# Performance work log

Hardware: AMD Instinct MI355X
Metric: run time of the kernel (lower is better)

Reference implementation:

```python
import jax, jax.numpy as jnp
import numpy as np


def _base_grid(B, H, W):
    xs = jnp.arange(W, dtype=jnp.float32)
    ys = jnp.arange(H, dtype=jnp.float32)
    gx, gy = jnp.meshgrid(xs, ys)  # [H,W] each, x varies along W
    return jnp.broadcast_to(jnp.stack([gx, gy], -1)[None], (B, H, W, 2))


def flow_to_grid(flow, accel=None):
    B, _, H, W = flow.shape
    v = 0.5 * flow
    if accel is not None:
        v = v + 0.25 * accel
    vgrid = _base_grid(B, H, W) + jnp.transpose(v, (0, 2, 3, 1))
    gx = 2.0 * vgrid[..., 0] / max(W - 1, 1) - 1.0
    gy = 2.0 * vgrid[..., 1] / max(H - 1, 1) - 1.0
    return jnp.stack([gx, gy], -1)  # [B,H,W,2]


def grid_sample_border(img, grid):
    # img [B,C,H,W], grid [B,Hg,Wg,2] normalized; bilinear, border pad, align_corners=True
    B, C, H, W = img.shape
    Hg, Wg = grid.shape[1], grid.shape[2]
    x = jnp.clip((grid[..., 0] + 1.0) * 0.5 * (W - 1), 0.0, W - 1)
    y = jnp.clip((grid[..., 1] + 1.0) * 0.5 * (H - 1), 0.0, H - 1)
    x0 = jnp.floor(x); y0 = jnp.floor(y)
    x1 = jnp.minimum(x0 + 1.0, W - 1); y1 = jnp.minimum(y0 + 1.0, H - 1)
    wx = (x - x0)[:, None]; wy = (y - y0)[:, None]  # [B,1,Hg,Wg]
    x0i, x1i, y0i, y1i = (a.astype(jnp.int32) for a in (x0, x1, y0, y1))
    flat = img.reshape(B, C, H * W)

    def gat(yi, xi):
        idx = jnp.broadcast_to((yi * W + xi).reshape(B, 1, Hg * Wg), (B, C, Hg * Wg))
        return jnp.take_along_axis(flat, idx, axis=2).reshape(B, C, Hg, Wg)

    v00, v01, v10, v11 = gat(y0i, x0i), gat(y0i, x1i), gat(y1i, x0i), gat(y1i, x1i)
    return v00 * (1 - wx) * (1 - wy) + v01 * wx * (1 - wy) + v10 * (1 - wx) * wy + v11 * wx * wy


def backward_warp(img, flow, accel=None):
    grid = flow_to_grid(flow, accel)
    warped = grid_sample_border(img, grid)
    valid = (jnp.abs(grid[..., 0]) <= 1.0) & (jnp.abs(grid[..., 1]) <= 1.0)
    return warped * valid[:, None].astype(img.dtype)


def local_kernel_warp(img, flow, kernel_params):
    B, C, H, W = img.shape
    k_row = jax.nn.softmax(kernel_params[:, :5], axis=1)   # [B,5,H,W]
    k_col = jax.nn.softmax(kernel_params[:, 5:10], axis=1)
    aniso = jax.nn.sigmoid(kernel_params[:, 10]) + 0.5     # [B,H,W]
    grid = flow_to_grid(flow)                               # [B,H,W,2]
    offsets = jnp.linspace(-2.0, 2.0, 5)
    a3 = aniso[..., None]                                   # [B,H,W,1]
    off_col = offsets.reshape(1, 1, 1, 5) * a3              # [B,H,W,5]
    off_row = offsets.reshape(1, 1, 1, 5) / a3
    zeros = jnp.zeros_like(off_row)
    grid_row = grid[:, :, :, None, :] + jnp.stack([off_row, zeros], -1) * (2.0 / W)
    samples_row = grid_sample_border(img, grid_row.reshape(B, H, W * 5, 2)).reshape(B, C, H, W, 5)
    img_row = jnp.einsum('bchwk,bkhw->bchw', samples_row, k_row)
    grid_base = flow_to_grid(jnp.zeros_like(flow))
    grid_col = grid_base[:, :, :, None, :] + jnp.stack([zeros, off_col], -1) * (2.0 / H)
    samples_col = grid_sample_border(img_row, grid_col.reshape(B, H, W * 5, 2)).reshape(B, C, H, W, 5)
    return jnp.einsum('bchwk,bkhw->bchw', samples_col, k_col)


def conv3x3(x, w, b):
    y = jax.lax.conv_general_dilated(x, w, (1, 1), 'SAME',
                                     dimension_numbers=('NCHW', 'OIHW', 'NCHW'))
    return y + b[None, :, None, None]


def reference(img, features, flow, kernel_params, w1, b1, w2, b2):
    B, _, H, W = img.shape
    Hf, Wf = features.shape[2], features.shape[3]
    warped_img = local_kernel_warp(img, flow, kernel_params)
    flow_scaled = jax.image.resize(flow, (B, 2, Hf, Wf), 'linear') * (Hf / H)
    warped_feat = backward_warp(features, flow_scaled)
    warped_img_down = jax.image.resize(warped_img, (B, 3, Hf, Wf), 'linear')
    x = jnp.concatenate([warped_feat, warped_img_down], axis=1)
    fused = conv3x3(jax.nn.relu(conv3x3(x, w1, b1)), w2, b2)
    return (warped_feat + fused, warped_img)


def setup_inputs() -> dict:
    key = jax.random.key(0)
    ks = jax.random.split(key, 6)
    B, H, W, Hf, Wf, Cf = 4, 512, 512, 256, 256, 96
    return {
        'img': jax.random.uniform(ks[0], (B, 3, H, W), jnp.float32),
        'features': jax.random.normal(ks[1], (B, Cf, Hf, Wf), jnp.float32),
        'flow': jax.random.normal(ks[2], (B, 2, H, W), jnp.float32) * 4.0,
        'kernel_params': jax.random.normal(ks[3], (B, 11, H, W), jnp.float32),
        'w1': jax.random.normal(ks[4], (Cf, Cf + 3, 3, 3), jnp.float32) * 0.02,
        'b1': jnp.zeros((Cf,), jnp.float32),
        'w2': jax.random.normal(ks[5], (Cf, Cf, 3, 3), jnp.float32) * 0.02,
        'b2': jnp.zeros((Cf,), jnp.float32),
    }
```

## Files before the change

kernel.cpp:

```cpp
#include <hip/hip_runtime.h>

#define NB 4
#define IH 512
#define IW 512
#define FH 256
#define FW 256
#define CF 96
#define C1 99
#define HWI (IH*IW)
#define HWF (FH*FW)

typedef short s8v __attribute__((ext_vector_type(8)));
typedef short s4v __attribute__((ext_vector_type(4)));
typedef float f4v __attribute__((ext_vector_type(4)));
typedef float f2v __attribute__((ext_vector_type(2), aligned(4)));

static __device__ __forceinline__ float sigmoidf_(float x) {
    return 1.0f / (1.0f + __expf(-x));
}
static __device__ __forceinline__ unsigned short f2bf(float f) {
    unsigned int u = __float_as_uint(f);
    unsigned int r = (u + 0x7fffu + ((u >> 16) & 1u)) >> 16;
    return (unsigned short)r;
}
static __device__ __forceinline__ float bf2f(short s) {
    unsigned int u = ((unsigned int)(unsigned short)s) << 16;
    return __uint_as_float(u);
}
static __device__ __forceinline__ void gl_lds16(const short* g, short* l) {
    __builtin_amdgcn_global_load_lds(
        (const __attribute__((address_space(1))) void*)g,
        (__attribute__((address_space(3))) void*)l, 16, 0, 0);
}

__global__ __launch_bounds__(256)
void lkw_row_kernel(const float* __restrict__ img,
                    const float* __restrict__ flow,
                    const float* __restrict__ kp,
                    float* __restrict__ img_row) {
    int idx = blockIdx.x * blockDim.x + threadIdx.x;
    if (idx >= NB * HWI) return;
    int w = idx & (IW - 1);
    int h = (idx >> 9) & (IH - 1);
    int b = idx >> 18;

    const float* kpb = kp + (size_t)b * 11 * HWI + h * IW + w;
    float p[5];
    float m = -1e30f;
    #pragma unroll
    for (int k = 0; k < 5; k++) { p[k] = kpb[k * HWI]; m = fmaxf(m, p[k]); }
    float s = 0.f;
    #pragma unroll
    for (int k = 0; k < 5; k++) { p[k] = __expf(p[k] - m); s += p[k]; }
    float invs = 1.f / s;
    float a = sigmoidf_(kpb[10 * HWI]) + 0.5f;
    float inva = 1.f / a;

    float fx = flow[((size_t)b * 2 + 0) * HWI + h * IW + w];
    float fy = flow[((size_t)b * 2 + 1) * HWI + h * IW + w];

    float y = (float)h + 0.5f * fy;
    y = fminf(fmaxf(y, 0.f), (float)(IH - 1));
    float y0f = floorf(y);
    int y0 = (int)y0f;
    int y1 = min(y0 + 1, IH - 1);
    float wy = y - y0f;

    float xbase = (float)w + 0.5f * fx;
    const float sc = (float)(IW - 1) / (float)IW;

    const float* imb = img + (size_t)b * 3 * HWI;
    float acc0 = 0.f, acc1 = 0.f, acc2 = 0.f;
    #pragma unroll
    for (int k = 0; k < 5; k++) {
        float x = xbase + (float)(k - 2) * inva * sc;
        x = fminf(fmaxf(x, 0.f), (float)(IW - 1));
        float x0f = floorf(x);
        int x0 = (int)x0f;
        int x1 = min(x0 + 1, IW - 1);
        float wx = x - x0f;
        float wk = p[k] * invs;
        float w00 = (1.f - wx) * (1.f - wy) * wk;
        float w01 = wx * (1.f - wy) * wk;
        float w10 = (1.f - wx) * wy * wk;
        float w11 = wx * wy * wk;
        int i00 = y0 * IW + x0, i01 = y0 * IW + x1;
        int i10 = y1 * IW + x0, i11 = y1 * IW + x1;
        acc0 += w00 * imb[i00] + w01 * imb[i01] + w10 * imb[i10] + w11 * imb[i11];
        acc1 += w00 * imb[HWI + i00] + w01 * imb[HWI + i01] + w10 * imb[HWI + i10] + w11 * imb[HWI + i11];
        acc2 += w00 * imb[2 * HWI + i00] + w01 * imb[2 * HWI + i01] + w10 * imb[2 * HWI + i10] + w11 * imb[2 * HWI + i11];
    }
    img_row[(size_t)b * 3 * HWI + h * IW + w] = acc0;
    img_row[(size_t)b * 3 * HWI + HWI + h * IW + w] = acc1;
    img_row[(size_t)b * 3 * HWI + 2 * HWI + h * IW + w] = acc2;
}

__global__ __launch_bounds__(256)
void lkw_col_kernel(const float* __restrict__ img_row,
                    const float* __restrict__ kp,
                    float* __restrict__ out1) {
    int idx = blockIdx.x * blockDim.x + threadIdx.x;
    if (idx >= NB * HWI) return;
    int w = idx & (IW - 1);
    int h = (idx >> 9) & (IH - 1);
    int b = idx >> 18;

    const float* kpb = kp + (size_t)b * 11 * HWI + h * IW + w;
    float p[5];
    float m = -1e30f;
    #pragma unroll
    for (int k = 0; k < 5; k++) { p[k] = kpb[(5 + k) * HWI]; m = fmaxf(m, p[k]); }
    float s = 0.f;
    #pragma unroll
    for (int k = 0; k < 5; k++) { p[k] = __expf(p[k] - m); s += p[k]; }
    float invs = 1.f / s;
    float a = sigmoidf_(kpb[10 * HWI]) + 0.5f;

    const float sc = (float)(IH - 1) / (float)IH;
    const float* irb = img_row + (size_t)b * 3 * HWI;
    float acc0 = 0.f, acc1 = 0.f, acc2 = 0.f;
    #pragma unroll
    for (int k = 0; k < 5; k++) {
        float y = (float)h + (float)(k - 2) * a * sc;
        y = fminf(fmaxf(y, 0.f), (float)(IH - 1));
        float y0f = floorf(y);
        int y0 = (int)y0f;
        int y1 = min(y0 + 1, IH - 1);
        float wy = y - y0f;
        float wk = p[k] * invs;
        float w0 = (1.f - wy) * wk, w1 = wy * wk;
        int i0 = y0 * IW + w, i1 = y1 * IW + w;
        acc0 += w0 * irb[i0] + w1 * irb[i1];
        acc1 += w0 * irb[HWI + i0] + w1 * irb[HWI + i1];
        acc2 += w0 * irb[2 * HWI + i0] + w1 * irb[2 * HWI + i1];
    }
    out1[(size_t)b * 3 * HWI + h * IW + w] = acc0;
    out1[(size_t)b * 3 * HWI + HWI + h * IW + w] = acc1;
    out1[(size_t)b * 3 * HWI + 2 * HWI + h * IW + w] = acc2;
}

static __device__ __forceinline__ void ds_taps(int i, int n_in, int t[4], float wt[4]) {
    int n_out = n_in >> 1;
    if (i == 0) {
        t[0] = 0; t[1] = 0; t[2] = 1; t[3] = 2;
        wt[0] = 0.f; wt[1] = 3.f / 7.f; wt[2] = 3.f / 7.f; wt[3] = 1.f / 7.f;
    } else if (i == n_out - 1) {
        t[0] = n_in - 3; t[1] = n_in - 2; t[2] = n_in - 1; t[3] = n_in - 1;
        wt[0] = 1.f / 7.f; wt[1] = 3.f / 7.f; wt[2] = 3.f / 7.f; wt[3] = 0.f;
    } else {
        t[0] = 2 * i - 1; t[1] = 2 * i; t[2] = 2 * i + 1; t[3] = 2 * i + 2;
        wt[0] = 0.125f; wt[1] = 0.375f; wt[2] = 0.375f; wt[3] = 0.125f;
    }
}

__global__ __launch_bounds__(256)
void downsample2x_kernel(const float* __restrict__ src, float* __restrict__ dst,
                         int BC, float mul) {
    int idx = blockIdx.x * blockDim.x + threadIdx.x;
    if (idx >= BC * HWF) return;
    int j = idx & (FW - 1);
    int i = (idx >> 8) & (FH - 1);
    int bc = idx >> 16;

    int tx[4], ty[4];
    float wx[4], wy[4];
    ds_taps(j, IW, tx, wx);
    ds_taps(i, IH, ty, wy);
    const float* s = src + (size_t)bc * HWI;
    float acc = 0.f;
    #pragma unroll
    for (int a = 0; a < 4; a++) {
        if (wy[a] == 0.f) continue;
        const float* rp = s + (size_t)ty[a] * IW;
        float row = wx[0] * rp[tx[0]] + wx[1] * rp[tx[1]] + wx[2] * rp[tx[2]] + wx[3] * rp[tx[3]];
        acc += wy[a] * row;
    }
    dst[idx] = acc * mul;
}

__global__ __launch_bounds__(256)
void imgdown_cl_kernel(const float* __restrict__ out1, short* __restrict__ xin) {
    int idx = blockIdx.x * blockDim.x + threadIdx.x;
    if (idx >= NB * HWF) return;
    int j = idx & (FW - 1);
    int i = (idx >> 8) & (FH - 1);
    int b = idx >> 16;

    int tx[4], ty[4];
    float wx[4], wy[4];
    ds_taps(j, IW, tx, wx);
    ds_taps(i, IH, ty, wy);
    const float* s = out1 + (size_t)b * 3 * HWI;
    float acc[3] = {0.f, 0.f, 0.f};
    #pragma unroll
    for (int a = 0; a < 4; a++) {
        if (wy[a] == 0.f) continue;
        #pragma unroll
        for (int c = 0; c < 3; c++) {
            const float* rp = s + (size_t)c * HWI + (size_t)ty[a] * IW;
            float row = wx[0] * rp[tx[0]] + wx[1] * rp[tx[1]] + wx[2] * rp[tx[2]] + wx[3] * rp[tx[3]];
            acc[c] += wy[a] * row;
        }
    }
    short* dst = xin + ((size_t)(b * FH + i) * FW + j) * 128 + 96;
    s8v g0 = { (short)f2bf(acc[0]), (short)f2bf(acc[1]), (short)f2bf(acc[2]), 0, 0, 0, 0, 0 };
    s8v z  = { 0, 0, 0, 0, 0, 0, 0, 0 };
    *(s8v*)(dst)      = g0;
    *(s8v*)(dst + 8)  = z;
    *(s8v*)(dst + 16) = z;
    *(s8v*)(dst + 24) = z;
}

template <int BF>
__global__ __launch_bounds__(256)
void feat_cl_kernel(const float* __restrict__ feat, void* __restrict__ featT) {
    __shared__ float tile[64 * 97];
    int blk = blockIdx.x;
    int b = blk >> 10;
    int p0 = (blk & 1023) << 6;
    int t = threadIdx.x;
    {
        int px = t & 63, cq = t >> 6;
        const float* src = feat + (size_t)b * CF * HWF + p0 + px;
        #pragma unroll
        for (int k = 0; k < 24; k++) {
            int c = cq * 24 + k;
            tile[px * 97 + c] = src[(size_t)c * HWF];
        }
    }
    __syncthreads();
    int pxo = t >> 2, co = (t & 3) * 24;
    const float* trow = &tile[pxo * 97 + co];
    size_t obase = ((size_t)(b * HWF) + p0 + pxo) * 96 + co;
    if (BF) {
        short* dst = (short*)featT + obase;
        #pragma unroll
        for (int q = 0; q < 3; q++) {
            s8v pk;
            #pragma unroll
            for (int e = 0; e < 8; e++) pk[e] = (short)f2bf(trow[q * 8 + e]);
            *(s8v*)(dst + q * 8) = pk;
        }
    } else {
        float* dst = (float*)featT + obase;
        #pragma unroll
        for (int q = 0; q < 6; q++) {
            f4v vv = { trow[q * 4 + 0], trow[q * 4 + 1], trow[q * 4 + 2], trow[q * 4 + 3] };
            *(f4v*)(dst + q * 4) = vv;
        }
    }
}

template <int BF>
__global__ __launch_bounds__(256)
void warp_feat_cl2_kernel(const void* __restrict__ featT,
                          const float* __restrict__ flow_s,
                          float* __restrict__ wfeat,
                          short* __restrict__ xin) {
    int t = blockIdx.x * 256 + threadIdx.x;
    int g = t & 7;
    int pix = t >> 3;
    int j = pix & (FW - 1);
    int i = (pix >> 8) & (FH - 1);
    int b = pix >> 16;

    float fx = flow_s[((size_t)b * 2 + 0) * HWF + i * FW + j];
    float fy = flow_s[((size_t)b * 2 + 1) * HWF + i * FW + j];
    float u = (float)j + 0.5f * fx;
    float v = (float)i + 0.5f * fy;
    bool valid = (u >= 0.f) && (u <= (float)(FW - 1)) && (v >= 0.f) && (v <= (float)(FH - 1));
    float x = fminf(fmaxf(u, 0.f), (float)(FW - 1));
    float y = fminf(fmaxf(v, 0.f), (float)(FH - 1));
    int x0 = min((int)x, FW - 2);
    int y0 = min((int)y, FH - 2);
    float wxf = x - (float)x0, wyf = y - (float)y0;
    float w00 = (1.f - wxf) * (1.f - wyf), w01 = wxf * (1.f - wyf);
    float w10 = (1.f - wxf) * wyf, w11 = wxf * wyf;
    if (!valid) { w00 = w01 = w10 = w11 = 0.f; }

    size_t base = ((size_t)(b * HWF) + (size_t)y0 * FW + x0) * 96 + g * 12;
    float vals[12];
    if (BF) {
        const short* fp = (const short*)featT + base;
        #pragma unroll
        for (int q = 0; q < 3; q++) {
            s4v a0 = *(const s4v*)(fp + q * 4);
            s4v a1 = *(const s4v*)(fp + 96 + q * 4);
            s4v a2 = *(const s4v*)(fp + 96 * FW + q * 4);
            s4v a3 = *(const s4v*)(fp + 96 * FW + 96 + q * 4);
            #pragma unroll
            for (int e = 0; e < 4; e++)
                vals[q * 4 + e] = w00 * bf2f(a0[e]) + w01 * bf2f(a1[e])
                                + w10 * bf2f(a2[e]) + w11 * bf2f(a3[e]);
        }
    } else {
        const float* fp = (const float*)featT + base;
        #pragma unroll
        for (int q = 0; q < 3; q++) {
            f4v a0 = *(const f4v*)(fp + q * 4);
            f4v a1 = *(const f4v*)(fp + 96 + q * 4);
            f4v a2 = *(const f4v*)(fp + 96 * FW + q * 4);
            f4v a3 = *(const f4v*)(fp + 96 * FW + 96 + q * 4);
            #pragma unroll
            for (int e = 0; e < 4; e++)
                vals[q * 4 + e] = w00 * a0[e] + w01 * a1[e] + w10 * a2[e] + w11 * a3[e];
        }
    }

    float* ob = wfeat + ((size_t)b * CF + g * 12) * HWF + (size_t)i * FW + j;
    #pragma unroll
    for (int k = 0; k < 12; k++) ob[(size_t)k * HWF] = vals[k];

    short* xr = xin + (size_t)pix * 128 + g * 12;
    #pragma unroll
    for (int q2 = 0; q2 < 3; q2++) {
        s4v pk = { (short)f2bf(vals[q2 * 4 + 0]), (short)f2bf(vals[q2 * 4 + 1]),
                   (short)f2bf(vals[q2 * 4 + 2]), (short)f2bf(vals[q2 * 4 + 3]) };
        *(s4v*)(xr + q2 * 4) = pk;
    }
}

__global__ __launch_bounds__(256)
void warp_feat_cl_kernel(const float* __restrict__ feat,
                         const float* __restrict__ flow_s,
                         float* __restrict__ wfeat,
                         short* __restrict__ xin) {
    int t = blockIdx.x * 256 + threadIdx.x;
    int g = t & 7;
    int pix = t >> 3;
    int j = pix & (FW - 1);
    int i = (pix >> 8) & (FH - 1);
    int b = pix >> 16;

    float fx = flow_s[((size_t)b * 2 + 0) * HWF + i * FW + j];
    float fy = flow_s[((size_t)b * 2 + 1) * HWF + i * FW + j];
    float u = (float)j + 0.5f * fx;
    float v = (float)i + 0.5f * fy;
    bool valid = (u >= 0.f) && (u <= (float)(FW - 1)) && (v >= 0.f) && (v <= (float)(FH - 1));
    float x = fminf(fmaxf(u, 0.f), (float)(FW - 1));
    float y = fminf(fmaxf(v, 0.f), (float)(FH - 1));
    int x0 = min((int)x, FW - 2);
    int y0 = min((int)y, FH - 2);
    float wxf = x - (float)x0, wyf = y - (float)y0;
    float w00 = (1.f - wxf) * (1.f - wyf), w01 = wxf * (1.f - wyf);
    float w10 = (1.f - wxf) * wyf, w11 = wxf * wyf;
    if (!valid) { w00 = w01 = w10 = w11 = 0.f; }

    const float* fb = feat + ((size_t)b * CF + g * 12) * HWF + (size_t)y0 * FW + x0;
    float vals[12];
    #pragma unroll
    for (int k = 0; k < 12; k++) {
        const float* p = fb + (size_t)k * HWF;
        f2v r0 = *(const f2v*)p;
        f2v r1 = *(const f2v*)(p + FW);
        vals[k] = w00 * r0.x + w01 * r0.y + w10 * r1.x + w11 * r1.y;
    }

    float* ob = wfeat + ((size_t)b * CF + g * 12) * HWF + (size_t)i * FW + j;
    #pragma unroll
    for (int k = 0; k < 12; k++) ob[(size_t)k * HWF] = vals[k];

    short* xr = xin + (size_t)pix * 128 + g * 12;
    #pragma unroll
    for (int q2 = 0; q2 < 3; q2++) {
        s4v pk = { (short)f2bf(vals[q2 * 4 + 0]), (short)f2bf(vals[q2 * 4 + 1]),
                   (short)f2bf(vals[q2 * 4 + 2]), (short)f2bf(vals[q2 * 4 + 3]) };
        *(s4v*)(xr + q2 * 4) = pk;
    }
}

__global__ __launch_bounds__(256)
void cvt_w1_kernel(const float* __restrict__ w1, short* __restrict__ wA1,
                   short* __restrict__ zpage) {
    int i = blockIdx.x * 256 + threadIdx.x;
    if (i < 128) zpage[i] = 0;
    if (i >= 4 * 3 * 3 * 96 * 32) return;
    int cl = i & 31;
    int co = (i >> 5) % 96;
    int rest = i / 3072;
    int dx = rest % 3;
    int dy = (rest / 3) % 3;
    int kc = rest / 9;
    int ci = kc * 32 + cl;
    float v = (ci < C1) ? w1[((size_t)co * C1 + ci) * 9 + dy * 3 + dx] : 0.f;
    wA1[i] = (short)f2bf(v);
}
__global__ __launch_bounds__(256)
void cvt_w2_kernel(const float* __restrict__ w2, short* __restrict__ wA2) {
    int i = blockIdx.x * 256 + threadIdx.x;
    if (i >= 3 * 3 * 3 * 96 * 32) return;
    int cl = i & 31;
    int co = (i >> 5) % 96;
    int rest = i / 3072;
    int dx = rest % 3;
    int dy = (rest / 3) % 3;
    int kc = rest / 9;
    wA2[i] = (short)f2bf(w2[((size_t)co * CF + kc * 32 + cl) * 9 + dy * 3 + dx]);
}

template <int PASS>
__global__ __launch_bounds__(256)
void conv_mfma4_kernel(const short* __restrict__ X,
                       const short* __restrict__ W,
                       const float* __restrict__ bias,
                       const short* __restrict__ zpage,
                       short* __restrict__ t1out,
                       float* __restrict__ out0) {
    constexpr int KSTR = (PASS == 1) ? 128 : 96;
    constexpr int KC = KSTR / 32;
    __shared__ short Als[320 * 32];
    __shared__ short Bls[192 * 32];

    const int bx = blockIdx.x;
    const int w0 = (bx & 1) * 128;
    const int h  = (bx >> 1) & (FH - 1);
    const int b  = bx >> 9;

    const int tid = threadIdx.x;
    const int lane = tid & 63;
    const int wv = tid >> 6;
    const int ln = lane & 15;
    const int q  = lane >> 4;

    f4v acc[6][2];
    #pragma unroll
    for (int mt = 0; mt < 6; mt++)
        #pragma unroll
        for (int nt = 0; nt < 2; nt++)
            acc[mt][nt] = (f4v){0.f, 0.f, 0.f, 0.f};

    const short* Xb = X + (size_t)(b * FH) * FW * KSTR;
    const int bpx = wv * 48 + (lane >> 2);
    const int bch = lane & 3;

    for (int kc = 0; kc < KC; ++kc) {
        for (int dy = 0; dy < 3; ++dy) {
            const int step = kc * 3 + dy;
            const int hy = h + dy - 1;
            const bool hok = (hy >= 0) && (hy < FH);
            const short* Xrow = Xb + (size_t)(hok ? hy : 0) * FW * KSTR + kc * 32;
            const short* Wstep = W + (size_t)step * 288 * 32;

            __syncthreads();
            #pragma unroll
            for (int k = 0; k < 5; k++) {
                int c = k * 4 + wv;
                const short* g = (c < 18) ? (Wstep + c * 512 + lane * 8) : zpage;
                gl_lds16(g, Als + c * 512);
            }
            #pragma unroll
            for (int k = 0; k < 3; k++) {
                int px = bpx + k * 16;
                int wp = w0 - 1 + px;
                bool ok = hok && (px < 130) && (wp >= 0) && (wp < FW);
                const short* g = ok ? (Xrow + (size_t)wp * KSTR + bch * 8) : zpage;
                gl_lds16(g, Bls + (wv * 48 + k * 16) * 32);
            }
            __syncthreads();

            #pragma unroll
            for (int dx = 0; dx < 3; ++dx) {
                s8v bfr0 = *(const s8v*)(Bls + (wv * 32 + ln + dx) * 32 + q * 8);
                s8v bfr1 = *(const s8v*)(Bls + (wv * 32 + 16 + ln + dx) * 32 + q * 8);
                #pragma unroll
                for (int mt = 0; mt < 6; ++mt) {
                    s8v afr = *(const s8v*)(Als + (dx * 96 + mt * 16 + ln) * 32 + q * 8);
                    acc[mt][0] = __builtin_amdgcn_mfma_f32_16x16x32_bf16(afr, bfr0, acc[mt][0], 0, 0, 0);
                    acc[mt][1] = __builtin_amdgcn_mfma_f32_16x16x32_bf16(afr, bfr1, acc[mt][1], 0, 0, 0);
                }
            }
        }
    }

    if (PASS == 1) {
        const size_t rowbase = (size_t)(b * FH + h) * FW;
        #pragma unroll
        for (int nt = 0; nt < 2; ++nt) {
            int pos = w0 + wv * 32 + nt * 16 + ln;
            short* dst = t1out + (rowbase + pos) * CF;
            #pragma unroll
            for (int mt = 0; mt < 6; ++mt) {
                int co0 = mt * 16 + q * 4;
                s4v pk;
                #pragma unroll
                for (int r = 0; r < 4; ++r) {
                    float v = acc[mt][nt][r] + bias[co0 + r];
                    pk[r] = (short)f2bf(fmaxf(v, 0.f));
                }
                *(s4v*)(dst + co0) = pk;
            }
        }
    } else {
        #pragma unroll
        for (int nt = 0; nt < 2; ++nt) {
            int pos = w0 + wv * 32 + nt * 16 + ln;
            #pragma unroll
            for (int mt = 0; mt < 6; ++mt) {
                int co0 = mt * 16 + q * 4;
                #pragma unroll
                for (int r = 0; r < 4; ++r) {
                    size_t o = (size_t)(b * CF + co0 + r) * HWF + (size_t)h * FW + pos;
                    out0[o] += acc[mt][nt][r] + bias[co0 + r];
                }
            }
        }
    }
}

extern "C" void kernel_launch(void* const* d_in, const int* in_sizes, int n_in,
                              void* d_out, int out_size, void* d_ws, size_t ws_size,
                              hipStream_t stream) {
    const float* img  = (const float*)d_in[0];
    const float* feat = (const float*)d_in[1];
    const float* flow = (const float*)d_in[2];
    const float* kp   = (const float*)d_in[3];
    const float* w1   = (const float*)d_in[4];
    const float* b1   = (const float*)d_in[5];
    const float* w2   = (const float*)d_in[6];
    const float* b2   = (const float*)d_in[7];

    float* out0 = (float*)d_out;
    float* out1 = out0 + (size_t)NB * CF * HWF;

    char* wsb = (char*)d_ws;
    short* wA1 = (short*)wsb;
    short* wA2 = (short*)(wsb + 221184);
    short* zpage = (short*)(wsb + 387072);
    short* xin = (short*)(wsb + 387328);
    const size_t off_after_xin = 387328 + 67108864;

    const size_t FEATT_F32 = (size_t)NB * HWF * 96 * 4;
    const size_t FEATT_BF16 = (size_t)NB * HWF * 96 * 2;
    const size_t FLOW_B = 2097152;
    const size_t need_f32 = off_after_xin + FLOW_B + FEATT_F32;
    const size_t need_b16 = off_after_xin + FLOW_B + FEATT_BF16;

    int n_img = NB * HWI;
    hipLaunchKernelGGL(cvt_w1_kernel, dim3((9 * 96 * 128 + 255) / 256), dim3(256), 0, stream, w1, wA1, zpage);
    hipLaunchKernelGGL(cvt_w2_kernel, dim3((9 * 96 * 96 + 255) / 256), dim3(256), 0, stream, w2, wA2);

    if (ws_size >= need_b16) {
        const bool f32ok = (ws_size >= need_f32);
        float* flow_s = (float*)(wsb + off_after_xin);
        char* region  = wsb + off_after_xin + FLOW_B;
        float* img_row = (float*)region;
        void*  featT   = (void*)region;
        short* t1cl    = (short*)region;

        hipLaunchKernelGGL(lkw_row_kernel, dim3((n_img + 255) / 256), dim3(256), 0, stream,
                           img, flow, kp, img_row);
        hipLaunchKernelGGL(lkw_col_kernel, dim3((n_img + 255) / 256), dim3(256), 0, stream,
                           img_row, kp, out1);
        hipLaunchKernelGGL(downsample2x_kernel, dim3((NB * 2 * HWF + 255) / 256), dim3(256), 0, stream,
                           flow, flow_s, NB * 2, 0.5f);
        hipLaunchKernelGGL(imgdown_cl_kernel, dim3((NB * HWF + 255) / 256), dim3(256), 0, stream,
                           out1, xin);
        if (f32ok) {
            hipLaunchKernelGGL((feat_cl_kernel<0>), dim3(NB * (HWF / 64)), dim3(256), 0, stream,
                               feat, featT);
            hipLaunchKernelGGL((warp_feat_cl2_kernel<0>), dim3(NB * HWF * 8 / 256), dim3(256), 0, stream,
                               featT, flow_s, out0, xin);
        } else {
            hipLaunchKernelGGL((feat_cl_kernel<1>), dim3(NB * (HWF / 64)), dim3(256), 0, stream,
                               feat, featT);
            hipLaunchKernelGGL((warp_feat_cl2_kernel<1>), dim3(NB * HWF * 8 / 256), dim3(256), 0, stream,
                               featT, flow_s, out0, xin);
        }
        hipLaunchKernelGGL((conv_mfma4_kernel<1>), dim3(NB * FH * 2), dim3(256), 0, stream,
                           xin, wA1, b1, zpage, t1cl, (float*)nullptr);
        hipLaunchKernelGGL((conv_mfma4_kernel<2>), dim3(NB * FH * 2), dim3(256), 0, stream,
                           t1cl, wA2, b2, zpage, (short*)nullptr, out0);
    } else {
        char* region = wsb + off_after_xin;
        short* t1cl    = (short*)region;
        float* img_row = (float*)region;
        float* flow_s  = (float*)(region + 16777216);

        hipLaunchKernelGGL(lkw_row_kernel, dim3((n_img + 255) / 256), dim3(256), 0, stream,
                           img, flow, kp, img_row);
        hipLaunchKernelGGL(lkw_col_kernel, dim3((n_img + 255) / 256), dim3(256), 0, stream,
                           img_row, kp, out1);
        hipLaunchKernelGGL(downsample2x_kernel, dim3((NB * 2 * HWF + 255) / 256), dim3(256), 0, stream,
                           flow, flow_s, NB * 2, 0.5f);
        hipLaunchKernelGGL(imgdown_cl_kernel, dim3((NB * HWF + 255) / 256), dim3(256), 0, stream,
                           out1, xin);
        hipLaunchKernelGGL(warp_feat_cl_kernel, dim3(NB * HWF * 8 / 256), dim3(256), 0, stream,
                           feat, flow_s, out0, xin);
        hipLaunchKernelGGL((conv_mfma4_kernel<1>), dim3(NB * FH * 2), dim3(256), 0, stream,
                           xin, wA1, b1, zpage, t1cl, (float*)nullptr);
        hipLaunchKernelGGL((conv_mfma4_kernel<2>), dim3(NB * FH * 2), dim3(256), 0, stream,
                           t1cl, wA2, b2, zpage, (short*)nullptr, out0);
    }
}
```

Baseline: 606.1 us.

## Double-buffer LDS tiles in MFMA conv kernel to overlap loads with compute

Restructures the conv inner loop into a flattened step loop with two LDS buffers for weights and input rows. The next step's global-to-LDS loads are issued before computing the current step, with explicit vmcnt waits and raw barriers, and wave priority is raised during the MFMA section. This is meant to hide global load latency behind matrix math, at the cost of doubling LDS per block, which may lower occupancy.

```diff
diff --git a/kernel.cpp b/kernel.cpp
--- a/kernel.cpp
+++ b/kernel.cpp
@@ -400,7 +400,7 @@
 
 template <int PASS>
 __global__ __launch_bounds__(256)
-void conv_mfma4_kernel(const short* __restrict__ X,
+void conv_mfma5_kernel(const short* __restrict__ X,
                        const short* __restrict__ W,
                        const float* __restrict__ bias,
                        const short* __restrict__ zpage,
@@ -408,8 +408,9 @@
                        float* __restrict__ out0) {
     constexpr int KSTR = (PASS == 1) ? 128 : 96;
     constexpr int KC = KSTR / 32;
-    __shared__ short Als[320 * 32];
-    __shared__ short Bls[192 * 32];
+    constexpr int NSTEP = KC * 3;
+    __shared__ short Als[2][320 * 32];
+    __shared__ short Bls[2][192 * 32];
 
     const int bx = blockIdx.x;
     const int w0 = (bx & 1) * 128;
@@ -433,43 +434,57 @@
     const int bpx = wv * 48 + (lane >> 2);
     const int bch = lane & 3;
 
-    for (int kc = 0; kc < KC; ++kc) {
-        for (int dy = 0; dy < 3; ++dy) {
-            const int step = kc * 3 + dy;
-            const int hy = h + dy - 1;
-            const bool hok = (hy >= 0) && (hy < FH);
-            const short* Xrow = Xb + (size_t)(hok ? hy : 0) * FW * KSTR + kc * 32;
-            const short* Wstep = W + (size_t)step * 288 * 32;
-
-            __syncthreads();
+    auto issue = [&](int s) {
+        const int kcn = s / 3, dyn = s - kcn * 3;
+        const int bufn = s & 1;
+        const int hy = h + dyn - 1;
+        const bool hok = (hy >= 0) && (hy < FH);
+        const short* Xrow = Xb + (size_t)(hok ? hy : 0) * FW * KSTR + kcn * 32;
+        const short* Wstep = W + (size_t)s * 288 * 32;
+        #pragma unroll
+        for (int k = 0; k < 5; k++) {
+            int c = k * 4 + wv;
+            const short* g = (c < 18) ? (Wstep + c * 512 + lane * 8) : zpage;
+            gl_lds16(g, &Als[bufn][c * 512]);
+        }
+        #pragma unroll
+        for (int k = 0; k < 3; k++) {
+            int px = bpx + k * 16;
+            int wp = w0 - 1 + px;
+            bool ok = hok && (px < 130) && (wp >= 0) && (wp < FW);
+            const short* g = ok ? (Xrow + (size_t)wp * KSTR + bch * 8) : zpage;
+            gl_lds16(g, &Bls[bufn][(wv * 48 + k * 16) * 32]);
+        }
+    };
+
+    issue(0);
+    for (int s = 0; s < NSTEP; ++s) {
+        if (s + 1 < NSTEP) {
+            issue(s + 1);
+            asm volatile("s_waitcnt vmcnt(8)" ::: "memory");
+        } else {
+            asm volatile("s_waitcnt vmcnt(0)" ::: "memory");
+        }
+        __builtin_amdgcn_s_barrier();
+        asm volatile("" ::: "memory");
+
+        const short* Ab = &Als[s & 1][0];
+        const short* Bb = &Bls[s & 1][0];
+        __builtin_amdgcn_s_setprio(1);
+        #pragma unroll
+        for (int dx = 0; dx < 3; ++dx) {
+            s8v bfr0 = *(const s8v*)(Bb + (wv * 32 + ln + dx) * 32 + q * 8);
+            s8v bfr1 = *(const s8v*)(Bb + (wv * 32 + 16 + ln + dx) * 32 + q * 8);
             #pragma unroll
-            for (int k = 0; k < 5; k++) {
-                int c = k * 4 + wv;
-                const short* g = (c < 18) ? (Wstep + c * 512 + lane * 8) : zpage;
-                gl_lds16(g, Als + c * 512);
+            for (int mt = 0; mt < 6; ++mt) {
+                s8v afr = *(const s8v*)(Ab + (dx * 96 + mt * 16 + ln) * 32 + q * 8);
+                acc[mt][0] = __builtin_amdgcn_mfma_f32_16x16x32_bf16(afr, bfr0, acc[mt][0], 0, 0, 0);
+                acc[mt][1] = __builtin_amdgcn_mfma_f32_16x16x32_bf16(afr, bfr1, acc[mt][1], 0, 0, 0);
             }
-            #pragma unroll
-            for (int k = 0; k < 3; k++) {
-                int px = bpx + k * 16;
-                int wp = w0 - 1 + px;
-                bool ok = hok && (px < 130) && (wp >= 0) && (wp < FW);
-                const short* g = ok ? (Xrow + (size_t)wp * KSTR + bch * 8) : zpage;
-                gl_lds16(g, Bls + (wv * 48 + k * 16) * 32);
-            }
-            __syncthreads();
-
-            #pragma unroll
-            for (int dx = 0; dx < 3; ++dx) {
-                s8v bfr0 = *(const s8v*)(Bls + (wv * 32 + ln + dx) * 32 + q * 8);
-                s8v bfr1 = *(const s8v*)(Bls + (wv * 32 + 16 + ln + dx) * 32 + q * 8);
-                #pragma unroll
-                for (int mt = 0; mt < 6; ++mt) {
-                    s8v afr = *(const s8v*)(Als + (dx * 96 + mt * 16 + ln) * 32 + q * 8);
-                    acc[mt][0] = __builtin_amdgcn_mfma_f32_16x16x32_bf16(afr, bfr0, acc[mt][0], 0, 0, 0);
-                    acc[mt][1] = __builtin_amdgcn_mfma_f32_16x16x32_bf16(afr, bfr1, acc[mt][1], 0, 0, 0);
-                }
-            }
-        }
+        }
+        __builtin_amdgcn_s_setprio(0);
+        asm volatile("" ::: "memory");
+        __builtin_amdgcn_s_barrier();
     }
 
     if (PASS == 1) {
@@ -566,9 +581,9 @@
             hipLaunchKernelGGL((warp_feat_cl2_kernel<1>), dim3(NB * HWF * 8 / 256), dim3(256), 0, stream,
                                featT, flow_s, out0, xin);
         }
-        hipLaunchKernelGGL((conv_mfma4_kernel<1>), dim3(NB * FH * 2), dim3(256), 0, stream,
+        hipLaunchKernelGGL((conv_mfma5_kernel<1>), dim3(NB * FH * 2), dim3(256), 0, stream,
                            xin, wA1, b1, zpage, t1cl, (float*)nullptr);
-        hipLaunchKernelGGL((conv_mfma4_kernel<2>), dim3(NB * FH * 2), dim3(256), 0, stream,
+        hipLaunchKernelGGL((conv_mfma5_kernel<2>), dim3(NB * FH * 2), dim3(256), 0, stream,
                            t1cl, wA2, b2, zpage, (short*)nullptr, out0);
     } else {
         char* region = wsb + off_after_xin;
@@ -586,9 +601,9 @@
                            out1, xin);
         hipLaunchKernelGGL(warp_feat_cl_kernel, dim3(NB * HWF * 8 / 256), dim3(256), 0, stream,
                            feat, flow_s, out0, xin);
-        hipLaunchKernelGGL((conv_mfma4_kernel<1>), dim3(NB * FH * 2), dim3(256), 0, stream,
+        hipLaunchKernelGGL((conv_mfma5_kernel<1>), dim3(NB * FH * 2), dim3(256), 0, stream,
                            xin, wA1, b1, zpage, t1cl, (float*)nullptr);
-        hipLaunchKernelGGL((conv_mfma4_kernel<2>), dim3(NB * FH * 2), dim3(256), 0, stream,
+        hipLaunchKernelGGL((conv_mfma5_kernel<2>), dim3(NB * FH * 2), dim3(256), 0, stream,
                            t1cl, wA2, b2, zpage, (short*)nullptr, out0);
     }
 }
```

New measurement: 580.5 us. 1.04x faster.
